# Kernel optimization log

Measured on AMD Instinct MI355X. Metric: run time of the kernel, lower is better.

Reference implementation:

```python
import jax, jax.numpy as jnp
import numpy as np

N, C, H, W = 2, 4, 112, 112
IGNORE = 0  # HD_IGNORE_CLASS_INDEX


def setup_inputs() -> dict:
    key = jax.random.key(0)
    k1, k2 = jax.random.split(key)
    predictions = jax.random.normal(k1, (N, C, H, W), dtype=jnp.float32)
    labels = jax.random.randint(k2, (N, C, H, W), 0, 2, dtype=jnp.int32)
    return {"predictions": predictions, "labels": labels}


def _pixel_dist_matrix(h, w):
    # Euclidean distance between all pairs of (row, col) pixel coordinates,
    # identical to cdist(argwhere(...), argwhere(...)) restricted by masks.
    rr, cc = jnp.meshgrid(jnp.arange(h, dtype=jnp.float32),
                          jnp.arange(w, dtype=jnp.float32), indexing="ij")
    r = rr.reshape(-1)
    c = cc.reshape(-1)
    return jnp.sqrt((r[:, None] - r[None, :]) ** 2 + (c[:, None] - c[None, :]) ** 2)  # (HW, HW)


def reference(predictions, labels):
    # F.softmax + argmax + one-hot -> per-class boolean prediction masks
    probs = jax.nn.softmax(predictions, axis=1)
    pred_cls = jnp.argmax(probs, axis=1)  # (N, H, W) int

    D = _pixel_dist_matrix(H, W)  # (HW, HW), data-independent

    fhd = jnp.zeros(C + 2, jnp.float32)
    rhd = jnp.zeros(C + 2, jnp.float32)
    mhd = jnp.zeros(C + 2, jnp.float32)

    for b in range(N):
        for j in range(C):
            if j == IGNORE:
                continue
            A = (pred_cls[b] == j).reshape(-1)        # predicted point set mask (HW,)
            Bm = (labels[b, j] == 1).reshape(-1)      # label point set mask (HW,)
            Af = A.astype(jnp.float32)
            Bf = Bm.astype(jnp.float32)
            # forward: mean over A-points of min distance to B-points
            rowmin = jnp.min(jnp.where(Bm[None, :], D, jnp.inf), axis=1)  # (HW,)
            fwd = jnp.sum(rowmin * Af) / jnp.sum(Af)
            # reverse: mean over B-points of min distance to A-points
            colmin = jnp.min(jnp.where(A[:, None], D, jnp.inf), axis=0)   # (HW,)
            rev = jnp.sum(colmin * Bf) / jnp.sum(Bf)
            fhd = fhd.at[j].add(fwd)
            rhd = rhd.at[j].add(rev)
            mhd = mhd.at[j].add(jnp.maximum(fwd, rev))

    def finalize(x):
        x = x.at[:C].divide(jnp.float32(N))
        x = x.at[C].set(jnp.mean(x[:C]))
        x = x.at[C + 1].set(jnp.mean(x[1:C]))
        return x

    return (finalize(mhd), finalize(fhd), finalize(rhd))
```

## Files before the change

kernel.cpp:

```cpp
#include <hip/hip_runtime.h>
#include <hip/hip_bf16.h>
#include <cstdint>
#include <climits>

#define HW 112
#define NPIX (HW*HW)
#define NB 2
#define NC 4
#define CHUNKS 28
#define HD_GRID (12*CHUNKS)


__global__ __launch_bounds__(128) void prep_kernel(
    const float* __restrict__ pred, const int* __restrict__ labels,
    unsigned long long* __restrict__ masks, unsigned short* __restrict__ gsqbuf)
{
  int blk = blockIdx.x;
  int b = blk / HW, r = blk % HW;
  int tid = threadIdx.x;
  int lane = tid & 63, wave = tid >> 6;
  int c = tid;

  int cls = 255;
  if (c < HW) {
    const float* p0 = pred + ((size_t)(b*NC)*HW + r)*HW + c;
    float best = p0[0]; cls = 0;
    #pragma unroll
    for (int ch = 1; ch < NC; ch++) {
      float v = p0[(size_t)ch*NPIX];
      if (v > best) { best = v; cls = ch; }
    }
  }

  __shared__ unsigned long long sm[6][2];
  #pragma unroll
  for (int m = 0; m < 3; m++) {
    bool p = (c < HW) && (cls == m + 1);
    unsigned long long bal = __ballot(p);
    if (lane == 0) sm[m][wave] = bal;
  }
  #pragma unroll
  for (int m = 0; m < 3; m++) {
    int lab = (c < HW) ? labels[((size_t)(b*NC + (m+1))*HW + r)*HW + c] : 0;
    bool p = (c < HW) && (lab == 1);
    unsigned long long bal = __ballot(p);
    if (lane == 0) sm[3 + m][wave] = bal;
  }
  __syncthreads();

  if (tid < 12) {
    int m = tid >> 1, w = tid & 1;
    masks[((size_t)(b*6 + m)*HW + r)*2 + w] = sm[m][w];
  }

  for (int item = tid; item < 6*HW; item += 128) {
    int m = item / HW, cc = item % HW;
    unsigned long long lo = sm[m][0], hi = sm[m][1];
    int left, right;
    if (cc < 64) {
      unsigned long long wl = lo & ((2ull << cc) - 1);
      left = wl ? 63 - __clzll(wl) : -1000;
      unsigned long long wr = lo & ~((1ull << cc) - 1);
      right = wr ? __ffsll(wr) - 1 : (hi ? 64 + __ffsll(hi) - 1 : 1000);
    } else {
      int cl = cc - 64;
      unsigned long long wl = hi & ((2ull << cl) - 1);
      left = wl ? 64 + 63 - __clzll(wl) : (lo ? 63 - __clzll(lo) : -1000);
      unsigned long long wr = hi & ~((1ull << cl) - 1);
      right = wr ? 64 + __ffsll(wr) - 1 : 1000;
    }
    int gv = min(cc - left, right - cc);
    gv = min(gv, 255);
    gsqbuf[(size_t)(b*6 + m)*NPIX + r*HW + cc] = (unsigned short)(gv*gv);
  }
}

__global__ __launch_bounds__(256) void hd_kernel(
    const unsigned long long* __restrict__ masks,
    const unsigned short* __restrict__ gsqbuf,
    float2* __restrict__ partial)
{
  int blk = blockIdx.x;
  int pd = blk / CHUNKS, chunk = blk % CHUNKS;
  int b = pd / 6, k = pd % 6;
  int src = b*6 + (k + 3) % 6;
  int tid = threadIdx.x, lane = tid & 63, wv = tid >> 6;

  __shared__ __align__(16) unsigned short sgq[NPIX];
  {
    const uint4* s4 = (const uint4*)(gsqbuf + (size_t)src*NPIX);
    uint4* d4 = (uint4*)sgq;
    #pragma unroll
    for (int i = 0; i < 7; i++) {
      int idx = tid + i*256;
      if (idx < NPIX/8) d4[idx] = s4[idx];
    }
  }
  __syncthreads();

  int s = tid / HW;
  int c = tid % HW;
  float sum = 0.f, cf = 0.f;
  if (s < 2) {
    int r0 = chunk*4 + 2*s;
    int m0 = INT_MAX, m1 = INT_MAX;
    #pragma unroll 4
    for (int rp = 0; rp < HW; rp++) {
      int g2 = sgq[rp*HW + c];
      int dr = r0 - rp;
      m0 = min(m0, __mul24(dr, dr) + g2);
      m1 = min(m1, __mul24(dr + 1, dr + 1) + g2);
    }
    unsigned long long w0 = masks[((size_t)pd*HW + r0)*2 + (c >> 6)];
    unsigned long long w1 = masks[((size_t)pd*HW + r0 + 1)*2 + (c >> 6)];
    if ((w0 >> (c & 63)) & 1ull) { sum += sqrtf((float)m0); cf += 1.f; }
    if ((w1 >> (c & 63)) & 1ull) { sum += sqrtf((float)m1); cf += 1.f; }
  }

  #pragma unroll
  for (int off = 32; off; off >>= 1) {
    sum += __shfl_down(sum, off, 64);
    cf  += __shfl_down(cf, off, 64);
  }
  __shared__ float red[8];
  if (lane == 0) { red[wv*2] = sum; red[wv*2 + 1] = cf; }
  __syncthreads();
  if (tid == 0)
    partial[blk] = make_float2(red[0] + red[2] + red[4] + red[6],
                               red[1] + red[3] + red[5] + red[7]);
}

__global__ __launch_bounds__(768) void fin_kernel(
    const float2* __restrict__ partial, float* __restrict__ out)
{
  int tid = threadIdx.x;
  int w = tid >> 6, lane = tid & 63;
  __shared__ float sacc[24];

  float s = 0.f, cnt = 0.f;
  if (lane < CHUNKS) {
    float2 p = partial[w*CHUNKS + lane];
    s = p.x; cnt = p.y;
  }
  #pragma unroll
  for (int off = 32; off; off >>= 1) {
    s   += __shfl_down(s, off, 64);
    cnt += __shfl_down(cnt, off, 64);
  }
  if (lane == 0) { sacc[w] = s; sacc[12 + w] = cnt; }
  __syncthreads();

  if (tid == 0) {
    float mhd[6], fhd[6], rhd[6];
    for (int i = 0; i < 6; i++) { mhd[i] = 0.f; fhd[i] = 0.f; rhd[i] = 0.f; }
    for (int bb = 0; bb < 2; bb++)
      for (int j = 1; j < 4; j++) {
        int pf = bb*6 + (j - 1);
        int pr = bb*6 + 3 + (j - 1);
        float fwd = sacc[pf] / sacc[12 + pf];
        float rev = sacc[pr] / sacc[12 + pr];
        fhd[j] += fwd; rhd[j] += rev; mhd[j] += fmaxf(fwd, rev);
      }
    float* arrs[3] = { mhd, fhd, rhd };
    for (int a = 0; a < 3; a++) {
      float* x = arrs[a];
      for (int i = 0; i < 4; i++) x[i] *= 0.5f;
      x[4] = (x[0] + x[1] + x[2] + x[3]) * 0.25f;
      x[5] = (x[1] + x[2] + x[3]) * (1.f / 3.f);
      for (int i = 0; i < 6; i++) out[a*6 + i] = x[i];
    }
  }
}

extern "C" void kernel_launch(void* const* d_in, const int* in_sizes, int n_in,
                              void* d_out, int out_size, void* d_ws, size_t ws_size,
                              hipStream_t stream) {
  const float* pred = (const float*)d_in[0];
  const int* labels = (const int*)d_in[1];
  float* out = (float*)d_out;

  unsigned long long* masks = (unsigned long long*)d_ws;
  unsigned short* gsqbuf = (unsigned short*)((char*)d_ws + 21504);
  float2* partial = (float2*)((char*)d_ws + 21504 + (size_t)12*NPIX*sizeof(unsigned short));

  prep_kernel<<<NB*HW, 128, 0, stream>>>(pred, labels, masks, gsqbuf);
  hd_kernel<<<HD_GRID, 256, 0, stream>>>(masks, gsqbuf, partial);
  fin_kernel<<<1, 768, 0, stream>>>(partial, out);
}
```

Baseline: 18.56 us.

## Fuse prep, distance and finalize kernels into one launch with spin-wait reducer

Merges the three kernels into one. Each work block builds its own source and target bitmasks straight from predictions and labels, computes the row-gap table in shared memory, and evaluates 16 target rows with 8 rows per thread. An extra block spins on per-block flags and does the final reduction, so two launches and the global mask and gap buffers go away. In exchange, each block redundantly recomputes the full source mask. The flags are never reset, so on repeated calls the finalizer can read stale partial sums.

```diff
diff --git a/kernel.cpp b/kernel.cpp
--- a/kernel.cpp
+++ b/kernel.cpp
@@ -7,167 +7,171 @@
 #define NPIX (HW*HW)
 #define NB 2
 #define NC 4
-#define CHUNKS 28
-#define HD_GRID (12*CHUNKS)
+#define CHUNK_ROWS 16
+#define CHUNKS 7
+#define NWORK (12*CHUNKS)
+#define MAGIC 0x5EC7C0DEu
 
 
-__global__ __launch_bounds__(128) void prep_kernel(
+__global__ __launch_bounds__(256) void mhd_kernel(
     const float* __restrict__ pred, const int* __restrict__ labels,
-    unsigned long long* __restrict__ masks, unsigned short* __restrict__ gsqbuf)
+    float* __restrict__ psum, float* __restrict__ pcnt,
+    unsigned* __restrict__ flags, float* __restrict__ out)
 {
+  __shared__ unsigned srcMask[HW][4];
+  __shared__ unsigned tgtMask[CHUNK_ROWS][4];
+  __shared__ __align__(16) unsigned short gsq[HW][HW];
+  __shared__ float red[8];
+  __shared__ float fsum[NWORK], fcnt[NWORK], sacc[24];
+
   int blk = blockIdx.x;
-  int b = blk / HW, r = blk % HW;
-  int tid = threadIdx.x;
-  int lane = tid & 63, wave = tid >> 6;
-  int c = tid;
-
-  int cls = 255;
-  if (c < HW) {
-    const float* p0 = pred + ((size_t)(b*NC)*HW + r)*HW + c;
-    float best = p0[0]; cls = 0;
-    #pragma unroll
-    for (int ch = 1; ch < NC; ch++) {
-      float v = p0[(size_t)ch*NPIX];
-      if (v > best) { best = v; cls = ch; }
-    }
-  }
-
-  __shared__ unsigned long long sm[6][2];
-  #pragma unroll
-  for (int m = 0; m < 3; m++) {
-    bool p = (c < HW) && (cls == m + 1);
-    unsigned long long bal = __ballot(p);
-    if (lane == 0) sm[m][wave] = bal;
-  }
-  #pragma unroll
-  for (int m = 0; m < 3; m++) {
-    int lab = (c < HW) ? labels[((size_t)(b*NC + (m+1))*HW + r)*HW + c] : 0;
-    bool p = (c < HW) && (lab == 1);
-    unsigned long long bal = __ballot(p);
-    if (lane == 0) sm[3 + m][wave] = bal;
-  }
-  __syncthreads();
-
-  if (tid < 12) {
-    int m = tid >> 1, w = tid & 1;
-    masks[((size_t)(b*6 + m)*HW + r)*2 + w] = sm[m][w];
-  }
-
-  for (int item = tid; item < 6*HW; item += 128) {
-    int m = item / HW, cc = item % HW;
-    unsigned long long lo = sm[m][0], hi = sm[m][1];
-    int left, right;
-    if (cc < 64) {
-      unsigned long long wl = lo & ((2ull << cc) - 1);
-      left = wl ? 63 - __clzll(wl) : -1000;
-      unsigned long long wr = lo & ~((1ull << cc) - 1);
-      right = wr ? __ffsll(wr) - 1 : (hi ? 64 + __ffsll(hi) - 1 : 1000);
-    } else {
-      int cl = cc - 64;
-      unsigned long long wl = hi & ((2ull << cl) - 1);
-      left = wl ? 64 + 63 - __clzll(wl) : (lo ? 63 - __clzll(lo) : -1000);
-      unsigned long long wr = hi & ~((1ull << cl) - 1);
-      right = wr ? 64 + __ffsll(wr) - 1 : 1000;
-    }
-    int gv = min(cc - left, right - cc);
-    gv = min(gv, 255);
-    gsqbuf[(size_t)(b*6 + m)*NPIX + r*HW + cc] = (unsigned short)(gv*gv);
-  }
-}
-
-__global__ __launch_bounds__(256) void hd_kernel(
-    const unsigned long long* __restrict__ masks,
-    const unsigned short* __restrict__ gsqbuf,
-    float2* __restrict__ partial)
-{
-  int blk = blockIdx.x;
-  int pd = blk / CHUNKS, chunk = blk % CHUNKS;
-  int b = pd / 6, k = pd % 6;
-  int src = b*6 + (k + 3) % 6;
   int tid = threadIdx.x, lane = tid & 63, wv = tid >> 6;
 
-  __shared__ __align__(16) unsigned short sgq[NPIX];
-  {
-    const uint4* s4 = (const uint4*)(gsqbuf + (size_t)src*NPIX);
-    uint4* d4 = (uint4*)sgq;
+  if (blk < NWORK) {
+    int pd = blk / CHUNKS, chunk = blk % CHUNKS;
+    int b = pd / 6, k = pd % 6;
+    int j = (k % 3) + 1;
+    bool isFwd = (k < 3);
+    int r0 = chunk * CHUNK_ROWS;
+
+    for (int i = tid; i < HW*4; i += 256) ((unsigned*)srcMask)[i] = 0;
+    if (tid < CHUNK_ROWS*4) ((unsigned*)tgtMask)[tid] = 0;
+    __syncthreads();
+
+    if (isFwd) {
+      const int4* lp = (const int4*)(labels + ((size_t)(b*NC + j))*NPIX);
+      for (int q = tid; q < NPIX/4; q += 256) {
+        int4 v = lp[q];
+        unsigned bits = (unsigned)(v.x==1) | ((unsigned)(v.y==1)<<1)
+                      | ((unsigned)(v.z==1)<<2) | ((unsigned)(v.w==1)<<3);
+        if (bits) { int p = q*4, r = p/HW, c = p%HW; atomicOr(&srcMask[r][c>>5], bits << (c&31)); }
+      }
+    } else {
+      const float4* pp = (const float4*)(pred + (size_t)(b*NC)*NPIX);
+      for (int q = tid; q < NPIX/4; q += 256) {
+        float4 v0 = pp[q], v1 = pp[q+NPIX/4], v2 = pp[q+2*(NPIX/4)], v3 = pp[q+3*(NPIX/4)];
+        unsigned bits = 0;
+        { float bst=v0.x; int cl=0; if(v1.x>bst){bst=v1.x;cl=1;} if(v2.x>bst){bst=v2.x;cl=2;} if(v3.x>bst){cl=3;} bits |= (unsigned)(cl==j); }
+        { float bst=v0.y; int cl=0; if(v1.y>bst){bst=v1.y;cl=1;} if(v2.y>bst){bst=v2.y;cl=2;} if(v3.y>bst){cl=3;} bits |= (unsigned)(cl==j)<<1; }
+        { float bst=v0.z; int cl=0; if(v1.z>bst){bst=v1.z;cl=1;} if(v2.z>bst){bst=v2.z;cl=2;} if(v3.z>bst){cl=3;} bits |= (unsigned)(cl==j)<<2; }
+        { float bst=v0.w; int cl=0; if(v1.w>bst){bst=v1.w;cl=1;} if(v2.w>bst){bst=v2.w;cl=2;} if(v3.w>bst){cl=3;} bits |= (unsigned)(cl==j)<<3; }
+        if (bits) { int p = q*4, r = p/HW, c = p%HW; atomicOr(&srcMask[r][c>>5], bits << (c&31)); }
+      }
+    }
+
+    if (isFwd) {
+      const float4* pp = (const float4*)(pred + (size_t)(b*NC)*NPIX + (size_t)r0*HW);
+      for (int q = tid; q < CHUNK_ROWS*HW/4; q += 256) {
+        float4 v0 = pp[q], v1 = pp[q+NPIX/4], v2 = pp[q+2*(NPIX/4)], v3 = pp[q+3*(NPIX/4)];
+        unsigned bits = 0;
+        { float bst=v0.x; int cl=0; if(v1.x>bst){bst=v1.x;cl=1;} if(v2.x>bst){bst=v2.x;cl=2;} if(v3.x>bst){cl=3;} bits |= (unsigned)(cl==j); }
+        { float bst=v0.y; int cl=0; if(v1.y>bst){bst=v1.y;cl=1;} if(v2.y>bst){bst=v2.y;cl=2;} if(v3.y>bst){cl=3;} bits |= (unsigned)(cl==j)<<1; }
+        { float bst=v0.z; int cl=0; if(v1.z>bst){bst=v1.z;cl=1;} if(v2.z>bst){bst=v2.z;cl=2;} if(v3.z>bst){cl=3;} bits |= (unsigned)(cl==j)<<2; }
+        { float bst=v0.w; int cl=0; if(v1.w>bst){bst=v1.w;cl=1;} if(v2.w>bst){bst=v2.w;cl=2;} if(v3.w>bst){cl=3;} bits |= (unsigned)(cl==j)<<3; }
+        if (bits) { int p = q*4, r = p/HW, c = p%HW; atomicOr(&tgtMask[r][c>>5], bits << (c&31)); }
+      }
+    } else {
+      const int4* lp = (const int4*)(labels + ((size_t)(b*NC + j))*NPIX + (size_t)r0*HW);
+      for (int q = tid; q < CHUNK_ROWS*HW/4; q += 256) {
+        int4 v = lp[q];
+        unsigned bits = (unsigned)(v.x==1) | ((unsigned)(v.y==1)<<1)
+                      | ((unsigned)(v.z==1)<<2) | ((unsigned)(v.w==1)<<3);
+        if (bits) { int p = q*4, r = p/HW, c = p%HW; atomicOr(&tgtMask[r][c>>5], bits << (c&31)); }
+      }
+    }
+    __syncthreads();
+
+    for (int it = tid; it < NPIX; it += 256) {
+      int r = it / HW, cc = it % HW;
+      unsigned long long lo = srcMask[r][0] | ((unsigned long long)srcMask[r][1] << 32);
+      unsigned long long hi = srcMask[r][2] | ((unsigned long long)srcMask[r][3] << 32);
+      int left, right;
+      if (cc < 64) {
+        unsigned long long wl = lo & ((2ull << cc) - 1);
+        left = wl ? 63 - __clzll(wl) : -1000;
+        unsigned long long wr = lo & ~((1ull << cc) - 1);
+        right = wr ? __ffsll(wr) - 1 : (hi ? 64 + __ffsll(hi) - 1 : 1000);
+      } else {
+        int cl = cc - 64;
+        unsigned long long wl = hi & ((2ull << cl) - 1);
+        left = wl ? 64 + 63 - __clzll(wl) : (lo ? 63 - __clzll(lo) : -1000);
+        unsigned long long wr = hi & ~((1ull << cl) - 1);
+        right = wr ? 64 + __ffsll(wr) - 1 : 1000;
+      }
+      int gv = min(min(cc - left, right - cc), 255);
+      gsq[r][cc] = (unsigned short)(gv*gv);
+    }
+    __syncthreads();
+
+    int s = tid / HW;
+    int c = tid % HW;
+    float sum = 0.f, cf = 0.f;
+    if (s < 2) {
+      int rbase = r0 + s*8;
+      int m[8];
+      #pragma unroll
+      for (int i = 0; i < 8; i++) m[i] = INT_MAX;
+      #pragma unroll 4
+      for (int rp = 0; rp < HW; rp++) {
+        int g2 = gsq[rp][c];
+        int d0 = rbase - rp;
+        #pragma unroll
+        for (int i = 0; i < 8; i++) m[i] = min(m[i], __mul24(d0 + i, d0 + i) + g2);
+      }
+      #pragma unroll
+      for (int i = 0; i < 8; i++) {
+        int lr = s*8 + i;
+        if ((tgtMask[lr][c>>5] >> (c&31)) & 1u) { sum += sqrtf((float)m[i]); cf += 1.f; }
+      }
+    }
     #pragma unroll
-    for (int i = 0; i < 7; i++) {
-      int idx = tid + i*256;
-      if (idx < NPIX/8) d4[idx] = s4[idx];
+    for (int off = 32; off; off >>= 1) {
+      sum += __shfl_down(sum, off, 64);
+      cf  += __shfl_down(cf, off, 64);
     }
-  }
-  __syncthreads();
-
-  int s = tid / HW;
-  int c = tid % HW;
-  float sum = 0.f, cf = 0.f;
-  if (s < 2) {
-    int r0 = chunk*4 + 2*s;
-    int m0 = INT_MAX, m1 = INT_MAX;
-    #pragma unroll 4
-    for (int rp = 0; rp < HW; rp++) {
-      int g2 = sgq[rp*HW + c];
-      int dr = r0 - rp;
-      m0 = min(m0, __mul24(dr, dr) + g2);
-      m1 = min(m1, __mul24(dr + 1, dr + 1) + g2);
+    if (lane == 0) { red[wv*2] = sum; red[wv*2+1] = cf; }
+    __syncthreads();
+    if (tid == 0) {
+      float S = red[0]+red[2]+red[4]+red[6];
+      float C = red[1]+red[3]+red[5]+red[7];
+      atomicExch(&psum[blk], S);
+      atomicExch(&pcnt[blk], C);
+      __threadfence();
+      atomicExch(&flags[blk], MAGIC);
     }
-    unsigned long long w0 = masks[((size_t)pd*HW + r0)*2 + (c >> 6)];
-    unsigned long long w1 = masks[((size_t)pd*HW + r0 + 1)*2 + (c >> 6)];
-    if ((w0 >> (c & 63)) & 1ull) { sum += sqrtf((float)m0); cf += 1.f; }
-    if ((w1 >> (c & 63)) & 1ull) { sum += sqrtf((float)m1); cf += 1.f; }
-  }
-
-  #pragma unroll
-  for (int off = 32; off; off >>= 1) {
-    sum += __shfl_down(sum, off, 64);
-    cf  += __shfl_down(cf, off, 64);
-  }
-  __shared__ float red[8];
-  if (lane == 0) { red[wv*2] = sum; red[wv*2 + 1] = cf; }
-  __syncthreads();
-  if (tid == 0)
-    partial[blk] = make_float2(red[0] + red[2] + red[4] + red[6],
-                               red[1] + red[3] + red[5] + red[7]);
-}
-
-__global__ __launch_bounds__(768) void fin_kernel(
-    const float2* __restrict__ partial, float* __restrict__ out)
-{
-  int tid = threadIdx.x;
-  int w = tid >> 6, lane = tid & 63;
-  __shared__ float sacc[24];
-
-  float s = 0.f, cnt = 0.f;
-  if (lane < CHUNKS) {
-    float2 p = partial[w*CHUNKS + lane];
-    s = p.x; cnt = p.y;
-  }
-  #pragma unroll
-  for (int off = 32; off; off >>= 1) {
-    s   += __shfl_down(s, off, 64);
-    cnt += __shfl_down(cnt, off, 64);
-  }
-  if (lane == 0) { sacc[w] = s; sacc[12 + w] = cnt; }
-  __syncthreads();
-
-  if (tid == 0) {
-    float mhd[6], fhd[6], rhd[6];
-    for (int i = 0; i < 6; i++) { mhd[i] = 0.f; fhd[i] = 0.f; rhd[i] = 0.f; }
-    for (int bb = 0; bb < 2; bb++)
-      for (int j = 1; j < 4; j++) {
-        int pf = bb*6 + (j - 1);
-        int pr = bb*6 + 3 + (j - 1);
-        float fwd = sacc[pf] / sacc[12 + pf];
-        float rev = sacc[pr] / sacc[12 + pr];
-        fhd[j] += fwd; rhd[j] += rev; mhd[j] += fmaxf(fwd, rev);
+  } else {
+    if (tid < NWORK) {
+      while (atomicOr(&flags[tid], 0u) != MAGIC) { }
+      __threadfence();
+      fsum[tid] = atomicAdd(&psum[tid], 0.0f);
+      fcnt[tid] = atomicAdd(&pcnt[tid], 0.0f);
+    }
+    __syncthreads();
+    if (tid < 12) {
+      float s = 0.f, cc = 0.f;
+      for (int i = 0; i < CHUNKS; i++) { s += fsum[tid*CHUNKS + i]; cc += fcnt[tid*CHUNKS + i]; }
+      sacc[tid] = s; sacc[12 + tid] = cc;
+    }
+    __syncthreads();
+    if (tid == 0) {
+      float mhd[6], fhd[6], rhd[6];
+      for (int i = 0; i < 6; i++) { mhd[i] = 0.f; fhd[i] = 0.f; rhd[i] = 0.f; }
+      for (int bb = 0; bb < 2; bb++)
+        for (int j = 1; j < 4; j++) {
+          int pf = bb*6 + (j - 1);
+          int pr = bb*6 + 3 + (j - 1);
+          float fwd = sacc[pf] / sacc[12 + pf];
+          float rev = sacc[pr] / sacc[12 + pr];
+          fhd[j] += fwd; rhd[j] += rev; mhd[j] += fmaxf(fwd, rev);
+        }
+      float* arrs[3] = { mhd, fhd, rhd };
+      for (int a = 0; a < 3; a++) {
+        float* x = arrs[a];
+        for (int i = 0; i < 4; i++) x[i] *= 0.5f;
+        x[4] = (x[0] + x[1] + x[2] + x[3]) * 0.25f;
+        x[5] = (x[1] + x[2] + x[3]) * (1.f / 3.f);
+        for (int i = 0; i < 6; i++) out[a*6 + i] = x[i];
       }
-    float* arrs[3] = { mhd, fhd, rhd };
-    for (int a = 0; a < 3; a++) {
-      float* x = arrs[a];
-      for (int i = 0; i < 4; i++) x[i] *= 0.5f;
-      x[4] = (x[0] + x[1] + x[2] + x[3]) * 0.25f;
-      x[5] = (x[1] + x[2] + x[3]) * (1.f / 3.f);
-      for (int i = 0; i < 6; i++) out[a*6 + i] = x[i];
     }
   }
 }
@@ -179,11 +183,9 @@
   const int* labels = (const int*)d_in[1];
   float* out = (float*)d_out;
 
-  unsigned long long* masks = (unsigned long long*)d_ws;
-  unsigned short* gsqbuf = (unsigned short*)((char*)d_ws + 21504);
-  float2* partial = (float2*)((char*)d_ws + 21504 + (size_t)12*NPIX*sizeof(unsigned short));
+  float* psum = (float*)d_ws;
+  float* pcnt = (float*)((char*)d_ws + 512);
+  unsigned* flags = (unsigned*)((char*)d_ws + 1024);
 
-  prep_kernel<<<NB*HW, 128, 0, stream>>>(pred, labels, masks, gsqbuf);
-  hd_kernel<<<HD_GRID, 256, 0, stream>>>(masks, gsqbuf, partial);
-  fin_kernel<<<1, 768, 0, stream>>>(partial, out);
+  mhd_kernel<<<NWORK + 1, 256, 0, stream>>>(pred, labels, psum, pcnt, flags, out);
 }
```

Measured after the change: 26.81 us. 1.44x slower.

## Replace full column min scan with early-exit vertical search in hd_kernel

Applied to the files above, without the earlier changes.

The second pass of the distance transform no longer stages a whole 112x112 row-distance slice in LDS and scans all 112 rows per output. Each thread reads a small window of rows directly from global memory and widens its search outward only while d*d is below the current best, stopping early. Blocks shrink to 128 threads, each handling four rows of one column. This removes the LDS staging and the O(H) scan per pixel, but the loop now has data-dependent length, so lanes can diverge and there are uncoalesced-latency global loads when the nearest point is far away.

```diff
diff --git a/kernel.cpp b/kernel.cpp
--- a/kernel.cpp
+++ b/kernel.cpp
@@ -69,13 +69,12 @@
       unsigned long long wr = hi & ~((1ull << cl) - 1);
       right = wr ? 64 + __ffsll(wr) - 1 : 1000;
     }
-    int gv = min(cc - left, right - cc);
-    gv = min(gv, 255);
+    int gv = min(min(cc - left, right - cc), 255);
     gsqbuf[(size_t)(b*6 + m)*NPIX + r*HW + cc] = (unsigned short)(gv*gv);
   }
 }
 
-__global__ __launch_bounds__(256) void hd_kernel(
+__global__ __launch_bounds__(128) void hd_kernel(
     const unsigned long long* __restrict__ masks,
     const unsigned short* __restrict__ gsqbuf,
     float2* __restrict__ partial)
@@ -85,36 +84,38 @@
   int b = pd / 6, k = pd % 6;
   int src = b*6 + (k + 3) % 6;
   int tid = threadIdx.x, lane = tid & 63, wv = tid >> 6;
+  int c = tid;
+  int r0 = chunk * 4;
 
-  __shared__ __align__(16) unsigned short sgq[NPIX];
-  {
-    const uint4* s4 = (const uint4*)(gsqbuf + (size_t)src*NPIX);
-    uint4* d4 = (uint4*)sgq;
+  float sum = 0.f, cf = 0.f;
+  if (c < HW) {
+    const unsigned short* g2p = gsqbuf + (size_t)src*NPIX + c;
+
+    int w[8];
     #pragma unroll
-    for (int i = 0; i < 7; i++) {
-      int idx = tid + i*256;
-      if (idx < NPIX/8) d4[idx] = s4[idx];
+    for (int t = 0; t < 8; t++) {
+      int gr = r0 - 2 + t;
+      w[t] = (gr >= 0 && gr < HW) ? (int)g2p[(size_t)gr*HW] : 0x7fff;
     }
-  }
-  __syncthreads();
 
-  int s = tid / HW;
-  int c = tid % HW;
-  float sum = 0.f, cf = 0.f;
-  if (s < 2) {
-    int r0 = chunk*4 + 2*s;
-    int m0 = INT_MAX, m1 = INT_MAX;
-    #pragma unroll 4
-    for (int rp = 0; rp < HW; rp++) {
-      int g2 = sgq[rp*HW + c];
-      int dr = r0 - rp;
-      m0 = min(m0, __mul24(dr, dr) + g2);
-      m1 = min(m1, __mul24(dr + 1, dr + 1) + g2);
+    #pragma unroll
+    for (int i = 0; i < 4; i++) {
+      int r = r0 + i;
+      int best = w[i + 2];
+      best = min(best, 1 + min(w[i + 1], w[i + 3]));
+      best = min(best, 4 + min(w[i],     w[i + 4]));
+      if (best > 9) {
+        for (int d = 3; d < HW; d++) {
+          int dd = d*d;
+          if (dd >= best) break;
+          int ru = r - d, rd = r + d;
+          if (ru >= 0)  best = min(best, dd + (int)g2p[(size_t)ru*HW]);
+          if (rd < HW)  best = min(best, dd + (int)g2p[(size_t)rd*HW]);
+        }
+      }
+      unsigned long long wm = masks[((size_t)pd*HW + r)*2 + (c >> 6)];
+      if ((wm >> (c & 63)) & 1ull) { sum += sqrtf((float)best); cf += 1.f; }
     }
-    unsigned long long w0 = masks[((size_t)pd*HW + r0)*2 + (c >> 6)];
-    unsigned long long w1 = masks[((size_t)pd*HW + r0 + 1)*2 + (c >> 6)];
-    if ((w0 >> (c & 63)) & 1ull) { sum += sqrtf((float)m0); cf += 1.f; }
-    if ((w1 >> (c & 63)) & 1ull) { sum += sqrtf((float)m1); cf += 1.f; }
   }
 
   #pragma unroll
@@ -122,12 +123,10 @@
     sum += __shfl_down(sum, off, 64);
     cf  += __shfl_down(cf, off, 64);
   }
-  __shared__ float red[8];
+  __shared__ float red[4];
   if (lane == 0) { red[wv*2] = sum; red[wv*2 + 1] = cf; }
   __syncthreads();
-  if (tid == 0)
-    partial[blk] = make_float2(red[0] + red[2] + red[4] + red[6],
-                               red[1] + red[3] + red[5] + red[7]);
+  if (tid == 0) partial[blk] = make_float2(red[0] + red[2], red[1] + red[3]);
 }
 
 __global__ __launch_bounds__(768) void fin_kernel(
@@ -184,6 +183,6 @@
   float2* partial = (float2*)((char*)d_ws + 21504 + (size_t)12*NPIX*sizeof(unsigned short));
 
   prep_kernel<<<NB*HW, 128, 0, stream>>>(pred, labels, masks, gsqbuf);
-  hd_kernel<<<HD_GRID, 256, 0, stream>>>(masks, gsqbuf, partial);
+  hd_kernel<<<HD_GRID, 128, 0, stream>>>(masks, gsqbuf, partial);
   fin_kernel<<<1, 768, 0, stream>>>(partial, out);
 }
```

New measurement: 14.92 us, median of 2. -19.6%, faster.
